# Kernel optimization log

Measured on AMD Instinct MI355X. Metric: run time of the kernel, lower is better.

The kernel has to match this reference:

```python
import jax, jax.numpy as jnp
import numpy as np

N, E = 50000, 800000
F_IN, HID, OUT, H = 128, 32, 4, 8
NEG_SLOPE = 0.2


def gat_conv(x, src, dst, W, a_src, a_dst, b):
    """PyG GATConv (concat=True, eval mode). x: [N,Fin]; src/dst: [E'] (self-loops included).
    W: [Fin, Hh*C]; a_src/a_dst: [Hh, C]; b: [Hh*C]."""
    n = x.shape[0]
    Hh, C = a_src.shape
    h = (x @ W).reshape(n, Hh, C)                      # [N,H,C]
    alpha_src = jnp.einsum('nhc,hc->nh', h, a_src)     # [N,H]
    alpha_dst = jnp.einsum('nhc,hc->nh', h, a_dst)     # [N,H]
    alpha = jax.nn.leaky_relu(alpha_src[src] + alpha_dst[dst], NEG_SLOPE)  # [E',H]
    # segment softmax over incoming edges of each dst node
    amax = jax.ops.segment_max(alpha, dst, num_segments=n)  # [N,H]
    ex = jnp.exp(alpha - amax[dst])
    denom = jax.ops.segment_sum(ex, dst, num_segments=n)    # [N,H]
    w = ex / (denom[dst] + 1e-16)                            # [E',H]
    msg = h[src] * w[:, :, None]                             # [E',H,C]
    out = jax.ops.segment_sum(msg, dst, num_segments=n)     # [N,H,C]
    return out.reshape(n, Hh * C) + b


def setup_inputs() -> dict:
    key = jax.random.key(0)
    ks = jax.random.split(key, 9)
    x = jax.random.normal(ks[0], (N, F_IN), jnp.float32)
    # random edge list without self loops (PyG GATConv removes then re-adds self loops)
    rng = np.random.default_rng(0)
    s = rng.integers(0, N, size=E)
    d = rng.integers(0, N, size=E)
    d = np.where(d == s, (d + 1) % N, d)
    edge_index = jnp.asarray(np.stack([s, d]), dtype=jnp.int32)
    g = lambda k, shape, fan: jax.random.normal(k, shape, jnp.float32) * (1.0 / np.sqrt(fan))
    W1 = g(ks[1], (F_IN, H * HID), F_IN)
    a_src1 = g(ks[2], (H, HID), HID)
    a_dst1 = g(ks[3], (H, HID), HID)
    b1 = jnp.zeros((H * HID,), jnp.float32)
    W2 = g(ks[4], (H * HID, H * OUT), H * HID)
    a_src2 = g(ks[5], (H, OUT), OUT)
    a_dst2 = g(ks[6], (H, OUT), OUT)
    b2 = jnp.zeros((H * OUT,), jnp.float32)
    return {"x": x, "edge_index": edge_index, "W1": W1, "a_src1": a_src1,
            "a_dst1": a_dst1, "b1": b1, "W2": W2, "a_src2": a_src2,
            "a_dst2": a_dst2, "b2": b2}


def reference(x, edge_index, W1, a_src1, a_dst1, b1, W2, a_src2, a_dst2, b2):
    n = x.shape[0]
    loops = jnp.arange(n, dtype=edge_index.dtype)
    src = jnp.concatenate([edge_index[0], loops])
    dst = jnp.concatenate([edge_index[1], loops])
    # layer 1 (dropout_edge / dropout are no-ops in eval mode)
    h = gat_conv(x, src, dst, W1, a_src1, a_dst1, b1)
    h = jax.nn.leaky_relu(h, NEG_SLOPE)
    # final layer (concat=True per the original code) -> [N, OUT*H]
    out = gat_conv(h, src, dst, W2, a_src2, a_dst2, b2)
    return out
```

## Files before the change

### kernel.cpp

```cpp
#include <hip/hip_runtime.h>
#include <hip/hip_bf16.h>
#include <cstdint>
#include <cstddef>


__device__ __forceinline__ float lrelu(float a) { return a > 0.f ? a : 0.2f * a; }

__device__ __forceinline__ unsigned short f2bf(float f) {
  unsigned u = __float_as_uint(f);
  unsigned r = (u + 0x7fff + ((u >> 16) & 1)) >> 16;
  return (unsigned short)r;
}
__device__ __forceinline__ float bf_lo(unsigned q) { return __uint_as_float(q << 16); }
__device__ __forceinline__ float bf_hi(unsigned q) { return __uint_as_float(q & 0xffff0000u); }

typedef __attribute__((ext_vector_type(8))) short bf16x8;
typedef __attribute__((ext_vector_type(4))) float f32x4;

#define ROWCAP 64


__global__ __launch_bounds__(256) void k_scatter(const int* __restrict__ srce,
                                                 const int* __restrict__ dste, int E, int n,
                                                 int* __restrict__ cursor,
                                                 int* __restrict__ srcs,
                                                 const float* __restrict__ W1,
                                                 unsigned short* __restrict__ W1T,
                                                 const float* __restrict__ W2,
                                                 unsigned short* __restrict__ W2T) {
  int t = blockIdx.x * 256 + threadIdx.x;
  if (t < E + n) {
    int s, d;
    if (t < E) { s = srce[t]; d = dste[t]; } else { s = d = t - E; }
    int pos = atomicAdd(&cursor[d], 1);
    srcs[(d << 6) + pos] = s;
  }
  if (t < 32768) {
    int k = t >> 8;
    int nn = t & 255;
    W1T[nn * 128 + k] = f2bf(W1[k * 256 + nn]);
  }
  if (t < 8192) {
    int k = t >> 5;
    int nn = t & 31;
    W2T[nn * 256 + k] = f2bf(W2[k * 32 + nn]);
  }
}


__global__ __launch_bounds__(256) void gemm1_mfma(const float* __restrict__ X,
                                                  const unsigned short* __restrict__ WT,
                                                  const float* __restrict__ a_src,
                                                  const float* __restrict__ a_dst,
                                                  unsigned short* __restrict__ h1,
                                                  float* __restrict__ a_s1,
                                                  float* __restrict__ a_d1,
                                                  int M) {
  __shared__ unsigned short As[64 * 136];
  __shared__ unsigned short Bs[256 * 72];
  const int row0 = blockIdx.x * 64;
  const int tid = threadIdx.x;
  const int wv = tid >> 6, lane = tid & 63;
  const int quad = lane >> 4, l15 = lane & 15;
  const int colw = wv * 64;

#pragma unroll
  for (int i = 0; i < 8; i++) {
    int j = tid + 256 * i;
    int r = j >> 5;
    int c4 = (j & 31) * 4;
    float4 v = make_float4(0.f, 0.f, 0.f, 0.f);
    if (row0 + r < M) v = *(const float4*)&X[(size_t)(row0 + r) * 128 + c4];
    uint2 p;
    p.x = (unsigned)f2bf(v.x) | ((unsigned)f2bf(v.y) << 16);
    p.y = (unsigned)f2bf(v.z) | ((unsigned)f2bf(v.w) << 16);
    *(uint2*)&As[r * 136 + c4] = p;
  }

  f32x4 acc[16];
#pragma unroll
  for (int i = 0; i < 16; i++) acc[i] = (f32x4)0.f;

  for (int kc = 0; kc < 128; kc += 64) {
    __syncthreads();
#pragma unroll
    for (int i = 0; i < 8; i++) {
      int j = tid + 256 * i;
      int nn = j >> 3;
      int kg = (j & 7) * 8;
      *(uint4*)&Bs[nn * 72 + kg] = *(const uint4*)&WT[nn * 128 + kc + kg];
    }
    __syncthreads();
#pragma unroll
    for (int ks = 0; ks < 64; ks += 32) {
      bf16x8 af[4], bfr[4];
#pragma unroll
      for (int mi = 0; mi < 4; mi++)
        af[mi] = *(const bf16x8*)&As[(mi * 16 + l15) * 136 + kc + ks + quad * 8];
#pragma unroll
      for (int ni = 0; ni < 4; ni++)
        bfr[ni] = *(const bf16x8*)&Bs[(colw + ni * 16 + l15) * 72 + ks + quad * 8];
#pragma unroll
      for (int mi = 0; mi < 4; mi++)
#pragma unroll
        for (int ni = 0; ni < 4; ni++)
          acc[mi * 4 + ni] = __builtin_amdgcn_mfma_f32_16x16x32_bf16(
              af[mi], bfr[ni], acc[mi * 4 + ni], 0, 0, 0);
    }
  }

  float as_[4], ad_[4];
#pragma unroll
  for (int ni = 0; ni < 4; ni++) {
    int nn = colw + ni * 16 + l15;
    as_[ni] = a_src[nn];
    ad_[ni] = a_dst[nn];
  }
  const int h0 = colw >> 5;
#pragma unroll
  for (int mi = 0; mi < 4; mi++) {
#pragma unroll
    for (int r = 0; r < 4; r++) {
      int m = row0 + mi * 16 + quad * 4 + r;
      bool valid = (m < M);
      if (valid) {
#pragma unroll
        for (int ni = 0; ni < 4; ni++)
          h1[(size_t)m * 256 + colw + ni * 16 + l15] = f2bf(acc[mi * 4 + ni][r]);
      }
      float s0 = fmaf(acc[mi * 4 + 0][r], as_[0], acc[mi * 4 + 1][r] * as_[1]);
      float s1 = fmaf(acc[mi * 4 + 2][r], as_[2], acc[mi * 4 + 3][r] * as_[3]);
      float d0 = fmaf(acc[mi * 4 + 0][r], ad_[0], acc[mi * 4 + 1][r] * ad_[1]);
      float d1 = fmaf(acc[mi * 4 + 2][r], ad_[2], acc[mi * 4 + 3][r] * ad_[3]);
#pragma unroll
      for (int mk = 1; mk <= 8; mk <<= 1) {
        s0 += __shfl_xor(s0, mk);
        s1 += __shfl_xor(s1, mk);
        d0 += __shfl_xor(d0, mk);
        d1 += __shfl_xor(d1, mk);
      }
      if (l15 == 0 && valid) {
        a_s1[m * 8 + h0]     = s0;
        a_s1[m * 8 + h0 + 1] = s1;
        a_d1[m * 8 + h0]     = d0;
        a_d1[m * 8 + h0 + 1] = d1;
      }
    }
  }
}


__global__ __launch_bounds__(256) void gemm2_mfma(const unsigned short* __restrict__ Xb,
                                                  const unsigned short* __restrict__ W2T,
                                                  const float* __restrict__ a_src,
                                                  const float* __restrict__ a_dst,
                                                  unsigned short* __restrict__ h2,
                                                  float* __restrict__ a_s2,
                                                  float* __restrict__ a_d2, int M) {
  __shared__ unsigned short As[64 * 264];
  __shared__ unsigned short Bs[32 * 264];
  const int row0 = blockIdx.x * 64;
  const int tid = threadIdx.x;
  const int wv = tid >> 6, lane = tid & 63;
  const int quad = lane >> 4, l15 = lane & 15;

#pragma unroll
  for (int i = 0; i < 8; i++) {
    int j = tid + 256 * i;
    int r = j >> 5;
    int c8 = (j & 31) * 8;
    uint4 v = make_uint4(0, 0, 0, 0);
    if (row0 + r < M) v = *(const uint4*)&Xb[(size_t)(row0 + r) * 256 + c8];
    *(uint4*)&As[r * 264 + c8] = v;
  }
#pragma unroll
  for (int i = 0; i < 4; i++) {
    int j = tid + 256 * i;
    int nn = j >> 5;
    int kg = (j & 31) * 8;
    *(uint4*)&Bs[nn * 264 + kg] = *(const uint4*)&W2T[nn * 256 + kg];
  }
  __syncthreads();

  f32x4 acc[2];
  acc[0] = (f32x4)0.f;
  acc[1] = (f32x4)0.f;
  const int mr = wv * 16;
#pragma unroll
  for (int ks = 0; ks < 256; ks += 32) {
    bf16x8 af = *(const bf16x8*)&As[(mr + l15) * 264 + ks + quad * 8];
    bf16x8 b0 = *(const bf16x8*)&Bs[(l15) * 264 + ks + quad * 8];
    bf16x8 b1 = *(const bf16x8*)&Bs[(16 + l15) * 264 + ks + quad * 8];
    acc[0] = __builtin_amdgcn_mfma_f32_16x16x32_bf16(af, b0, acc[0], 0, 0, 0);
    acc[1] = __builtin_amdgcn_mfma_f32_16x16x32_bf16(af, b1, acc[1], 0, 0, 0);
  }

  float as_[2], ad_[2];
#pragma unroll
  for (int ni = 0; ni < 2; ni++) {
    int c = ni * 16 + l15;
    as_[ni] = a_src[c];
    ad_[ni] = a_dst[c];
  }
#pragma unroll
  for (int r = 0; r < 4; r++) {
    int m = row0 + mr + quad * 4 + r;
    bool valid = (m < M);
    float s0 = acc[0][r] * as_[0];
    float s1 = acc[1][r] * as_[1];
    float d0 = acc[0][r] * ad_[0];
    float d1 = acc[1][r] * ad_[1];
#pragma unroll
    for (int mk = 1; mk <= 2; mk <<= 1) {
      s0 += __shfl_xor(s0, mk);
      s1 += __shfl_xor(s1, mk);
      d0 += __shfl_xor(d0, mk);
      d1 += __shfl_xor(d1, mk);
    }
    if (valid) {
      h2[(size_t)m * 32 + l15]      = f2bf(acc[0][r]);
      h2[(size_t)m * 32 + 16 + l15] = f2bf(acc[1][r]);
      if ((l15 & 3) == 0) {
        int hq = l15 >> 2;
        a_s2[m * 8 + hq]     = s0;
        a_s2[m * 8 + 4 + hq] = s1;
        a_d2[m * 8 + hq]     = d0;
        a_d2[m * 8 + 4 + hq] = d1;
      }
    }
  }
}


__global__ __launch_bounds__(256) void gat_agg_l1(const unsigned short* __restrict__ h,
                                                  const float* __restrict__ asrc,
                                                  const float* __restrict__ adst,
                                                  const int* __restrict__ rowcnt,
                                                  const int* __restrict__ srcs,
                                                  const float* __restrict__ bias,
                                                  unsigned short* __restrict__ out, int n) {
  int wave = threadIdx.x >> 6;
  int lane = threadIdx.x & 63;
  int d = blockIdx.x * 4 + wave;
  if (d >= n) return;
  int begin = d << 6;
  int end = begin + rowcnt[d];
  int hh = lane & 7;
  float ad = adst[d * 8 + hh];

  const int myhead = lane >> 3;
  float denom = 0.f;
  float4 acc0 = make_float4(0.f, 0.f, 0.f, 0.f);
  float4 acc1 = make_float4(0.f, 0.f, 0.f, 0.f);
#define ACCA(ff, qq)                                        \
    acc0.x = fmaf(ff, bf_lo(qq.x), acc0.x);                 \
    acc0.y = fmaf(ff, bf_hi(qq.x), acc0.y);                 \
    acc0.z = fmaf(ff, bf_lo(qq.y), acc0.z);                 \
    acc0.w = fmaf(ff, bf_hi(qq.y), acc0.w);
#define ACCB(ff, qq)                                        \
    acc1.x = fmaf(ff, bf_lo(qq.x), acc1.x);                 \
    acc1.y = fmaf(ff, bf_hi(qq.x), acc1.y);                 \
    acc1.z = fmaf(ff, bf_lo(qq.y), acc1.z);                 \
    acc1.w = fmaf(ff, bf_hi(qq.y), acc1.w);

  int e = begin;
  for (; e + 16 <= end; e += 16) {
    int s[16];
#pragma unroll
    for (int j = 0; j < 16; j++) s[j] = srcs[e + j];
    float w[16];
    if (lane < 8) {
#pragma unroll
      for (int j = 0; j < 16; j++) {
        w[j] = __expf(lrelu(asrc[s[j] * 8 + lane] + ad));
        denom += w[j];
      }
    } else {
#pragma unroll
      for (int j = 0; j < 16; j++) w[j] = 0.f;
    }
    uint2 q[16];
#pragma unroll
    for (int j = 0; j < 16; j++) q[j] = *(const uint2*)&h[(size_t)s[j] * 256 + lane * 4];
    float f[16];
#pragma unroll
    for (int j = 0; j < 16; j++) f[j] = __shfl(w[j], myhead);
#pragma unroll
    for (int j = 0; j < 16; j += 2) {
      ACCA(f[j], q[j])
      ACCB(f[j + 1], q[j + 1])
    }
  }
  for (; e < end; e += 8) {
    int s[8];
    float w[8];
#pragma unroll
    for (int j = 0; j < 8; j++) {
      int ee = e + j;
      s[j] = srcs[ee < end ? ee : end - 1];
    }
    if (lane < 8) {
#pragma unroll
      for (int j = 0; j < 8; j++) {
        float v = __expf(lrelu(asrc[s[j] * 8 + lane] + ad));
        w[j] = (e + j < end) ? v : 0.f;
        denom += w[j];
      }
    } else {
#pragma unroll
      for (int j = 0; j < 8; j++) w[j] = 0.f;
    }
    uint2 q[8];
#pragma unroll
    for (int j = 0; j < 8; j++) q[j] = *(const uint2*)&h[(size_t)s[j] * 256 + lane * 4];
    float f[8];
#pragma unroll
    for (int j = 0; j < 8; j++) f[j] = __shfl(w[j], myhead);
#pragma unroll
    for (int j = 0; j < 8; j += 2) {
      ACCA(f[j], q[j])
      ACCB(f[j + 1], q[j + 1])
    }
  }
#undef ACCA
#undef ACCB
  float4 acc;
  acc.x = acc0.x + acc1.x;
  acc.y = acc0.y + acc1.y;
  acc.z = acc0.z + acc1.z;
  acc.w = acc0.w + acc1.w;
  float dn = __shfl(denom, myhead) + 1e-16f;
  float inv = 1.f / dn;
  int f = lane * 4;
  float4 bv = *(const float4*)&bias[f];
  float rx = lrelu(acc.x * inv + bv.x);
  float ry = lrelu(acc.y * inv + bv.y);
  float rz = lrelu(acc.z * inv + bv.z);
  float rw = lrelu(acc.w * inv + bv.w);
  uint2 p;
  p.x = (unsigned)f2bf(rx) | ((unsigned)f2bf(ry) << 16);
  p.y = (unsigned)f2bf(rz) | ((unsigned)f2bf(rw) << 16);
  *(uint2*)&out[(size_t)d * 256 + f] = p;
}

__global__ __launch_bounds__(256) void gat_agg_l2(const unsigned short* __restrict__ h,
                                                  const float* __restrict__ asrc,
                                                  const float* __restrict__ adst,
                                                  const int* __restrict__ rowcnt,
                                                  const int* __restrict__ srcs,
                                                  const float* __restrict__ bias,
                                                  float* __restrict__ out, int n) {
  int wave = threadIdx.x >> 6;
  int lane = threadIdx.x & 63;
  int d = blockIdx.x * 4 + wave;
  if (d >= n) return;
  int begin = d << 6;
  int end = begin + rowcnt[d];
  int hh = lane & 7;
  int eg = lane >> 3;
  float ad = adst[d * 8 + hh];

  float denom = 0.f;
  float4 acc = make_float4(0.f, 0.f, 0.f, 0.f);
  for (int base = begin; base < end; base += 32) {
    int eA = base + eg;
    int eB = base + 8 + eg;
    int eC = base + 16 + eg;
    int eD = base + 24 + eg;
    bool vA = eA < end, vB = eB < end, vC = eC < end, vD = eD < end;
    int sA = srcs[vA ? eA : begin];
    int sB = srcs[vB ? eB : begin];
    int sC = srcs[vC ? eC : begin];
    int sD = srcs[vD ? eD : begin];
    float aA = asrc[sA * 8 + hh];
    float aB = asrc[sB * 8 + hh];
    float aC = asrc[sC * 8 + hh];
    float aD = asrc[sD * 8 + hh];
    uint2 qA = *(const uint2*)&h[(size_t)sA * 32 + hh * 4];
    uint2 qB = *(const uint2*)&h[(size_t)sB * 32 + hh * 4];
    uint2 qC = *(const uint2*)&h[(size_t)sC * 32 + hh * 4];
    uint2 qD = *(const uint2*)&h[(size_t)sD * 32 + hh * 4];
    float wA = vA ? __expf(lrelu(aA + ad)) : 0.f;
    float wB = vB ? __expf(lrelu(aB + ad)) : 0.f;
    float wC = vC ? __expf(lrelu(aC + ad)) : 0.f;
    float wD = vD ? __expf(lrelu(aD + ad)) : 0.f;
    denom += (wA + wB) + (wC + wD);
    acc.x = fmaf(wA, bf_lo(qA.x), acc.x); acc.y = fmaf(wA, bf_hi(qA.x), acc.y);
    acc.z = fmaf(wA, bf_lo(qA.y), acc.z); acc.w = fmaf(wA, bf_hi(qA.y), acc.w);
    acc.x = fmaf(wB, bf_lo(qB.x), acc.x); acc.y = fmaf(wB, bf_hi(qB.x), acc.y);
    acc.z = fmaf(wB, bf_lo(qB.y), acc.z); acc.w = fmaf(wB, bf_hi(qB.y), acc.w);
    acc.x = fmaf(wC, bf_lo(qC.x), acc.x); acc.y = fmaf(wC, bf_hi(qC.x), acc.y);
    acc.z = fmaf(wC, bf_lo(qC.y), acc.z); acc.w = fmaf(wC, bf_hi(qC.y), acc.w);
    acc.x = fmaf(wD, bf_lo(qD.x), acc.x); acc.y = fmaf(wD, bf_hi(qD.x), acc.y);
    acc.z = fmaf(wD, bf_lo(qD.y), acc.z); acc.w = fmaf(wD, bf_hi(qD.y), acc.w);
  }
#pragma unroll
  for (int mask = 8; mask <= 32; mask <<= 1) {
    denom += __shfl_xor(denom, mask);
    acc.x += __shfl_xor(acc.x, mask);
    acc.y += __shfl_xor(acc.y, mask);
    acc.z += __shfl_xor(acc.z, mask);
    acc.w += __shfl_xor(acc.w, mask);
  }
  if (lane < 8) {
    float inv = 1.f / (denom + 1e-16f);
    int f = lane * 4;
    float4 bv = *(const float4*)&bias[f];
    float4 r;
    r.x = acc.x * inv + bv.x;
    r.y = acc.y * inv + bv.y;
    r.z = acc.z * inv + bv.z;
    r.w = acc.w * inv + bv.w;
    *(float4*)&out[(size_t)d * 32 + f] = r;
  }
}


extern "C" void kernel_launch(void* const* d_in, const int* in_sizes, int n_in,
                              void* d_out, int out_size, void* d_ws, size_t ws_size,
                              hipStream_t stream) {
  const float* x   = (const float*)d_in[0];
  const int*   ei  = (const int*)d_in[1];
  const float* W1  = (const float*)d_in[2];
  const float* as1 = (const float*)d_in[3];
  const float* ad1 = (const float*)d_in[4];
  const float* b1  = (const float*)d_in[5];
  const float* W2  = (const float*)d_in[6];
  const float* as2 = (const float*)d_in[7];
  const float* ad2 = (const float*)d_in[8];
  const float* b2  = (const float*)d_in[9];
  float* out = (float*)d_out;

  const int E = in_sizes[1] / 2;
  const int n = in_sizes[0] / 128;
  const int* srce = ei;
  const int* dste = ei + E;

  char* ws = (char*)d_ws;
  size_t off = 0;
  auto alloc = [&](size_t bytes) -> void* {
    void* p = ws + off;
    off = (off + bytes + 255) & ~(size_t)255;
    return p;
  };
  int* cursor   = (int*)alloc((size_t)n * 4);
  int* srcs     = (int*)alloc((size_t)n * ROWCAP * 4);
  unsigned short* h1  = (unsigned short*)alloc((size_t)n * 256 * 2);
  unsigned short* w1t = (unsigned short*)alloc((size_t)256 * 128 * 2);
  unsigned short* w2t = (unsigned short*)alloc((size_t)32 * 256 * 2);
  float* a_s1   = (float*)alloc((size_t)n * 8 * 4);
  float* a_d1   = (float*)alloc((size_t)n * 8 * 4);
  unsigned short* x2 = (unsigned short*)alloc((size_t)n * 256 * 2);
  unsigned short* h2 = (unsigned short*)alloc((size_t)n * 32 * 2);
  float* a_s2   = (float*)alloc((size_t)n * 8 * 4);
  float* a_d2   = (float*)alloc((size_t)n * 8 * 4);

  const int tot = E + n;
  hipMemsetAsync(cursor, 0, (size_t)n * 4, stream);
  k_scatter<<<(tot + 255) / 256, 256, 0, stream>>>(srce, dste, E, n, cursor, srcs,
                                                   W1, w1t, W2, w2t);

  gemm1_mfma<<<(n + 63) / 64, 256, 0, stream>>>(x, w1t, as1, ad1, h1, a_s1, a_d1, n);
  gat_agg_l1<<<(n + 3) / 4, 256, 0, stream>>>(h1, a_s1, a_d1, cursor, srcs, b1, x2, n);

  gemm2_mfma<<<(n + 63) / 64, 256, 0, stream>>>(x2, w2t, as2, ad2, h2, a_s2, a_d2, n);
  gat_agg_l2<<<(n + 3) / 4, 256, 0, stream>>>(h2, a_s2, a_d2, cursor, srcs, b2, out, n);
}
```

Measured before the change: 266.8 us.

## Fuse layer-1 aggregation with layer-2 GEMM via shared-memory tile

Merges the layer-1 attention aggregation and the layer-2 MFMA GEMM into one kernel. Each wave aggregates 16 destination nodes in turn and writes the bf16 results straight into the shared-memory A tile, which the GEMM then consumes. This removes the global write and re-read of the intermediate feature matrix and one kernel launch. In exchange the grid shrinks from one node per wave to 64 nodes per block, and each block holds a large LDS footprint, which cuts the number of waves available to hide latency in the irregular gather.

Measured after the change: 305.8 us. +14.6%, slower.

```diff
diff --git a/kernel.cpp b/kernel.cpp
--- a/kernel.cpp
+++ b/kernel.cpp
@@ -150,108 +150,27 @@
 }
 
 
-__global__ __launch_bounds__(256) void gemm2_mfma(const unsigned short* __restrict__ Xb,
-                                                  const unsigned short* __restrict__ W2T,
-                                                  const float* __restrict__ a_src,
-                                                  const float* __restrict__ a_dst,
-                                                  unsigned short* __restrict__ h2,
-                                                  float* __restrict__ a_s2,
-                                                  float* __restrict__ a_d2, int M) {
-  __shared__ unsigned short As[64 * 264];
-  __shared__ unsigned short Bs[32 * 264];
-  const int row0 = blockIdx.x * 64;
-  const int tid = threadIdx.x;
-  const int wv = tid >> 6, lane = tid & 63;
-  const int quad = lane >> 4, l15 = lane & 15;
-
-#pragma unroll
-  for (int i = 0; i < 8; i++) {
-    int j = tid + 256 * i;
-    int r = j >> 5;
-    int c8 = (j & 31) * 8;
-    uint4 v = make_uint4(0, 0, 0, 0);
-    if (row0 + r < M) v = *(const uint4*)&Xb[(size_t)(row0 + r) * 256 + c8];
-    *(uint4*)&As[r * 264 + c8] = v;
-  }
-#pragma unroll
-  for (int i = 0; i < 4; i++) {
-    int j = tid + 256 * i;
-    int nn = j >> 5;
-    int kg = (j & 31) * 8;
-    *(uint4*)&Bs[nn * 264 + kg] = *(const uint4*)&W2T[nn * 256 + kg];
-  }
-  __syncthreads();
-
-  f32x4 acc[2];
-  acc[0] = (f32x4)0.f;
-  acc[1] = (f32x4)0.f;
-  const int mr = wv * 16;
-#pragma unroll
-  for (int ks = 0; ks < 256; ks += 32) {
-    bf16x8 af = *(const bf16x8*)&As[(mr + l15) * 264 + ks + quad * 8];
-    bf16x8 b0 = *(const bf16x8*)&Bs[(l15) * 264 + ks + quad * 8];
-    bf16x8 b1 = *(const bf16x8*)&Bs[(16 + l15) * 264 + ks + quad * 8];
-    acc[0] = __builtin_amdgcn_mfma_f32_16x16x32_bf16(af, b0, acc[0], 0, 0, 0);
-    acc[1] = __builtin_amdgcn_mfma_f32_16x16x32_bf16(af, b1, acc[1], 0, 0, 0);
-  }
-
-  float as_[2], ad_[2];
-#pragma unroll
-  for (int ni = 0; ni < 2; ni++) {
-    int c = ni * 16 + l15;
-    as_[ni] = a_src[c];
-    ad_[ni] = a_dst[c];
-  }
-#pragma unroll
-  for (int r = 0; r < 4; r++) {
-    int m = row0 + mr + quad * 4 + r;
-    bool valid = (m < M);
-    float s0 = acc[0][r] * as_[0];
-    float s1 = acc[1][r] * as_[1];
-    float d0 = acc[0][r] * ad_[0];
-    float d1 = acc[1][r] * ad_[1];
-#pragma unroll
-    for (int mk = 1; mk <= 2; mk <<= 1) {
-      s0 += __shfl_xor(s0, mk);
-      s1 += __shfl_xor(s1, mk);
-      d0 += __shfl_xor(d0, mk);
-      d1 += __shfl_xor(d1, mk);
-    }
-    if (valid) {
-      h2[(size_t)m * 32 + l15]      = f2bf(acc[0][r]);
-      h2[(size_t)m * 32 + 16 + l15] = f2bf(acc[1][r]);
-      if ((l15 & 3) == 0) {
-        int hq = l15 >> 2;
-        a_s2[m * 8 + hq]     = s0;
-        a_s2[m * 8 + 4 + hq] = s1;
-        a_d2[m * 8 + hq]     = d0;
-        a_d2[m * 8 + 4 + hq] = d1;
-      }
-    }
-  }
-}
-
-
-__global__ __launch_bounds__(256) void gat_agg_l1(const unsigned short* __restrict__ h,
+__global__ __launch_bounds__(256) void agg1_gemm2(const unsigned short* __restrict__ h,
                                                   const float* __restrict__ asrc,
                                                   const float* __restrict__ adst,
                                                   const int* __restrict__ rowcnt,
                                                   const int* __restrict__ srcs,
                                                   const float* __restrict__ bias,
-                                                  unsigned short* __restrict__ out, int n) {
-  int wave = threadIdx.x >> 6;
-  int lane = threadIdx.x & 63;
-  int d = blockIdx.x * 4 + wave;
-  if (d >= n) return;
-  int begin = d << 6;
-  int end = begin + rowcnt[d];
-  int hh = lane & 7;
-  float ad = adst[d * 8 + hh];
-
+                                                  const unsigned short* __restrict__ W2T,
+                                                  const float* __restrict__ a_src2,
+                                                  const float* __restrict__ a_dst2,
+                                                  unsigned short* __restrict__ h2,
+                                                  float* __restrict__ a_s2,
+                                                  float* __restrict__ a_d2, int n) {
+  __shared__ unsigned short As[64 * 264];
+  __shared__ unsigned short Bs[32 * 264];
+  const int tid = threadIdx.x;
+  const int wv = tid >> 6, lane = tid & 63;
+  const int quad = lane >> 4, l15 = lane & 15;
+  const int d0 = blockIdx.x * 64;
+  const int hh = lane & 7;
   const int myhead = lane >> 3;
-  float denom = 0.f;
-  float4 acc0 = make_float4(0.f, 0.f, 0.f, 0.f);
-  float4 acc1 = make_float4(0.f, 0.f, 0.f, 0.f);
+
 #define ACCA(ff, qq)                                        \
     acc0.x = fmaf(ff, bf_lo(qq.x), acc0.x);                 \
     acc0.y = fmaf(ff, bf_hi(qq.x), acc0.y);                 \
@@ -263,85 +182,154 @@
     acc1.z = fmaf(ff, bf_lo(qq.y), acc1.z);                 \
     acc1.w = fmaf(ff, bf_hi(qq.y), acc1.w);
 
-  int e = begin;
-  for (; e + 16 <= end; e += 16) {
-    int s[16];
-#pragma unroll
-    for (int j = 0; j < 16; j++) s[j] = srcs[e + j];
-    float w[16];
-    if (lane < 8) {
-#pragma unroll
-      for (int j = 0; j < 16; j++) {
-        w[j] = __expf(lrelu(asrc[s[j] * 8 + lane] + ad));
-        denom += w[j];
-      }
-    } else {
-#pragma unroll
-      for (int j = 0; j < 16; j++) w[j] = 0.f;
-    }
-    uint2 q[16];
-#pragma unroll
-    for (int j = 0; j < 16; j++) q[j] = *(const uint2*)&h[(size_t)s[j] * 256 + lane * 4];
-    float f[16];
-#pragma unroll
-    for (int j = 0; j < 16; j++) f[j] = __shfl(w[j], myhead);
-#pragma unroll
-    for (int j = 0; j < 16; j += 2) {
-      ACCA(f[j], q[j])
-      ACCB(f[j + 1], q[j + 1])
-    }
-  }
-  for (; e < end; e += 8) {
-    int s[8];
-    float w[8];
-#pragma unroll
-    for (int j = 0; j < 8; j++) {
-      int ee = e + j;
-      s[j] = srcs[ee < end ? ee : end - 1];
-    }
-    if (lane < 8) {
+  float4 bv = *(const float4*)&bias[lane * 4];
+  for (int i = 0; i < 16; i++) {
+    int dl = wv * 16 + i;
+    int d = d0 + dl;
+    if (d >= n) break;
+    int begin = d << 6;
+    int end = begin + rowcnt[d];
+    float ad = adst[d * 8 + hh];
+
+    float denom = 0.f;
+    float4 acc0 = make_float4(0.f, 0.f, 0.f, 0.f);
+    float4 acc1 = make_float4(0.f, 0.f, 0.f, 0.f);
+    int e = begin;
+    for (; e + 16 <= end; e += 16) {
+      int s[16];
+#pragma unroll
+      for (int j = 0; j < 16; j++) s[j] = srcs[e + j];
+      float w[16];
+      if (lane < 8) {
+#pragma unroll
+        for (int j = 0; j < 16; j++) {
+          w[j] = __expf(lrelu(asrc[s[j] * 8 + lane] + ad));
+          denom += w[j];
+        }
+      } else {
+#pragma unroll
+        for (int j = 0; j < 16; j++) w[j] = 0.f;
+      }
+      uint2 q[16];
+#pragma unroll
+      for (int j = 0; j < 16; j++) q[j] = *(const uint2*)&h[(size_t)s[j] * 256 + lane * 4];
+      float f[16];
+#pragma unroll
+      for (int j = 0; j < 16; j++) f[j] = __shfl(w[j], myhead);
+#pragma unroll
+      for (int j = 0; j < 16; j += 2) {
+        ACCA(f[j], q[j])
+        ACCB(f[j + 1], q[j + 1])
+      }
+    }
+    for (; e < end; e += 8) {
+      int s[8];
+      float w[8];
 #pragma unroll
       for (int j = 0; j < 8; j++) {
-        float v = __expf(lrelu(asrc[s[j] * 8 + lane] + ad));
-        w[j] = (e + j < end) ? v : 0.f;
-        denom += w[j];
-      }
-    } else {
-#pragma unroll
-      for (int j = 0; j < 8; j++) w[j] = 0.f;
-    }
-    uint2 q[8];
-#pragma unroll
-    for (int j = 0; j < 8; j++) q[j] = *(const uint2*)&h[(size_t)s[j] * 256 + lane * 4];
-    float f[8];
-#pragma unroll
-    for (int j = 0; j < 8; j++) f[j] = __shfl(w[j], myhead);
-#pragma unroll
-    for (int j = 0; j < 8; j += 2) {
-      ACCA(f[j], q[j])
-      ACCB(f[j + 1], q[j + 1])
-    }
+        int ee = e + j;
+        s[j] = srcs[ee < end ? ee : end - 1];
+      }
+      if (lane < 8) {
+#pragma unroll
+        for (int j = 0; j < 8; j++) {
+          float v = __expf(lrelu(asrc[s[j] * 8 + lane] + ad));
+          w[j] = (e + j < end) ? v : 0.f;
+          denom += w[j];
+        }
+      } else {
+#pragma unroll
+        for (int j = 0; j < 8; j++) w[j] = 0.f;
+      }
+      uint2 q[8];
+#pragma unroll
+      for (int j = 0; j < 8; j++) q[j] = *(const uint2*)&h[(size_t)s[j] * 256 + lane * 4];
+      float f[8];
+#pragma unroll
+      for (int j = 0; j < 8; j++) f[j] = __shfl(w[j], myhead);
+#pragma unroll
+      for (int j = 0; j < 8; j += 2) {
+        ACCA(f[j], q[j])
+        ACCB(f[j + 1], q[j + 1])
+      }
+    }
+    float4 acc;
+    acc.x = acc0.x + acc1.x;
+    acc.y = acc0.y + acc1.y;
+    acc.z = acc0.z + acc1.z;
+    acc.w = acc0.w + acc1.w;
+    float dn = __shfl(denom, myhead) + 1e-16f;
+    float inv = 1.f / dn;
+    float rx = lrelu(acc.x * inv + bv.x);
+    float ry = lrelu(acc.y * inv + bv.y);
+    float rz = lrelu(acc.z * inv + bv.z);
+    float rw = lrelu(acc.w * inv + bv.w);
+    uint2 p;
+    p.x = (unsigned)f2bf(rx) | ((unsigned)f2bf(ry) << 16);
+    p.y = (unsigned)f2bf(rz) | ((unsigned)f2bf(rw) << 16);
+    *(uint2*)&As[dl * 264 + lane * 4] = p;
   }
 #undef ACCA
 #undef ACCB
-  float4 acc;
-  acc.x = acc0.x + acc1.x;
-  acc.y = acc0.y + acc1.y;
-  acc.z = acc0.z + acc1.z;
-  acc.w = acc0.w + acc1.w;
-  float dn = __shfl(denom, myhead) + 1e-16f;
-  float inv = 1.f / dn;
-  int f = lane * 4;
-  float4 bv = *(const float4*)&bias[f];
-  float rx = lrelu(acc.x * inv + bv.x);
-  float ry = lrelu(acc.y * inv + bv.y);
-  float rz = lrelu(acc.z * inv + bv.z);
-  float rw = lrelu(acc.w * inv + bv.w);
-  uint2 p;
-  p.x = (unsigned)f2bf(rx) | ((unsigned)f2bf(ry) << 16);
-  p.y = (unsigned)f2bf(rz) | ((unsigned)f2bf(rw) << 16);
-  *(uint2*)&out[(size_t)d * 256 + f] = p;
-}
+
+#pragma unroll
+  for (int i = 0; i < 4; i++) {
+    int j = tid + 256 * i;
+    int nn = j >> 5;
+    int kg = (j & 31) * 8;
+    *(uint4*)&Bs[nn * 264 + kg] = *(const uint4*)&W2T[nn * 256 + kg];
+  }
+  __syncthreads();
+
+  f32x4 acc2[2];
+  acc2[0] = (f32x4)0.f;
+  acc2[1] = (f32x4)0.f;
+  const int mr = wv * 16;
+#pragma unroll
+  for (int ks = 0; ks < 256; ks += 32) {
+    bf16x8 af = *(const bf16x8*)&As[(mr + l15) * 264 + ks + quad * 8];
+    bf16x8 b0 = *(const bf16x8*)&Bs[(l15) * 264 + ks + quad * 8];
+    bf16x8 b1 = *(const bf16x8*)&Bs[(16 + l15) * 264 + ks + quad * 8];
+    acc2[0] = __builtin_amdgcn_mfma_f32_16x16x32_bf16(af, b0, acc2[0], 0, 0, 0);
+    acc2[1] = __builtin_amdgcn_mfma_f32_16x16x32_bf16(af, b1, acc2[1], 0, 0, 0);
+  }
+
+  float as_[2], ad_[2];
+#pragma unroll
+  for (int ni = 0; ni < 2; ni++) {
+    int c = ni * 16 + l15;
+    as_[ni] = a_src2[c];
+    ad_[ni] = a_dst2[c];
+  }
+#pragma unroll
+  for (int r = 0; r < 4; r++) {
+    int m = d0 + mr + quad * 4 + r;
+    bool valid = (m < n);
+    float s0 = acc2[0][r] * as_[0];
+    float s1 = acc2[1][r] * as_[1];
+    float dd0 = acc2[0][r] * ad_[0];
+    float dd1 = acc2[1][r] * ad_[1];
+#pragma unroll
+    for (int mk = 1; mk <= 2; mk <<= 1) {
+      s0 += __shfl_xor(s0, mk);
+      s1 += __shfl_xor(s1, mk);
+      dd0 += __shfl_xor(dd0, mk);
+      dd1 += __shfl_xor(dd1, mk);
+    }
+    if (valid) {
+      h2[(size_t)m * 32 + l15]      = f2bf(acc2[0][r]);
+      h2[(size_t)m * 32 + 16 + l15] = f2bf(acc2[1][r]);
+      if ((l15 & 3) == 0) {
+        int hq = l15 >> 2;
+        a_s2[m * 8 + hq]     = s0;
+        a_s2[m * 8 + 4 + hq] = s1;
+        a_d2[m * 8 + hq]     = dd0;
+        a_d2[m * 8 + 4 + hq] = dd1;
+      }
+    }
+  }
+}
+
 
 __global__ __launch_bounds__(256) void gat_agg_l2(const unsigned short* __restrict__ h,
                                                   const float* __restrict__ asrc,
@@ -450,7 +438,6 @@
   unsigned short* w2t = (unsigned short*)alloc((size_t)32 * 256 * 2);
   float* a_s1   = (float*)alloc((size_t)n * 8 * 4);
   float* a_d1   = (float*)alloc((size_t)n * 8 * 4);
-  unsigned short* x2 = (unsigned short*)alloc((size_t)n * 256 * 2);
   unsigned short* h2 = (unsigned short*)alloc((size_t)n * 32 * 2);
   float* a_s2   = (float*)alloc((size_t)n * 8 * 4);
   float* a_d2   = (float*)alloc((size_t)n * 8 * 4);
@@ -461,8 +448,7 @@
                                                    W1, w1t, W2, w2t);
 
   gemm1_mfma<<<(n + 63) / 64, 256, 0, stream>>>(x, w1t, as1, ad1, h1, a_s1, a_d1, n);
-  gat_agg_l1<<<(n + 3) / 4, 256, 0, stream>>>(h1, a_s1, a_d1, cursor, srcs, b1, x2, n);
-
-  gemm2_mfma<<<(n + 63) / 64, 256, 0, stream>>>(x2, w2t, as2, ad2, h2, a_s2, a_d2, n);
+  agg1_gemm2<<<(n + 63) / 64, 256, 0, stream>>>(h1, a_s1, a_d1, cursor, srcs, b1,
+                                                w2t, as2, ad2, h2, a_s2, a_d2, n);
   gat_agg_l2<<<(n + 3) / 4, 256, 0, stream>>>(h2, a_s2, a_d2, cursor, srcs, b2, out, n);
 }
```
